# Performance work log

Hardware: AMD Instinct MI355X
Metric: run time of the kernel (lower is better)

Reference implementation:

```python
import jax, jax.numpy as jnp
import numpy as np

B, S, D, ENC_S = 4, 1024, 1024, 512
DI, DFF, DFE = 2048, 4096, 2048
NA, NB, E, H = 2, 6, 8, 16
TOP_K = 2


def setup_inputs():
    key = jax.random.key(0)
    ks = jax.random.split(key, 24)
    s = 0.02
    n = jax.random.normal
    return {
        "x": n(ks[0], (B, S, D), jnp.float32),
        "encoder_out": n(ks[1], (B, ENC_S, D), jnp.float32),
        "encoder_mask": jnp.ones((B, ENC_S), dtype=bool),
        "padding_mask": jnp.ones((B, S), dtype=bool),
        "encoder_available": jax.random.randint(ks[2], (B,), 0, 2, jnp.int32),
        "ln_g": jnp.ones((D,), jnp.float32),
        "ln_b": jnp.zeros((D,), jnp.float32),
        "ssm_Win": s * n(ks[3], (D, 2 * DI), jnp.float32),
        "ssm_a": n(ks[4], (DI,), jnp.float32),
        "ssm_Wout": s * n(ks[5], (DI, D), jnp.float32),
        "attn_Wqkv": s * n(ks[6], (D, 3 * D), jnp.float32),
        "attn_Wo": s * n(ks[7], (D, D), jnp.float32),
        "beta_ssm": 0.8 * jnp.ones((D,), jnp.float32),
        "beta_attn": 0.2 * jnp.ones((D,), jnp.float32),
        "se_W1": s * n(ks[8], (D, DFF), jnp.float32),
        "se_b1": jnp.zeros((DFF,), jnp.float32),
        "se_W2": s * n(ks[9], (DFF, D), jnp.float32),
        "se_b2": jnp.zeros((D,), jnp.float32),
        "r_W": s * n(ks[10], (D + 1, E), jnp.float32),
        "r_b": jnp.zeros((E,), jnp.float32),
        "ea_Wq": s * n(ks[11], (NA, D, D), jnp.float32),
        "ea_Wk": s * n(ks[12], (NA, D, D), jnp.float32),
        "ea_Wv": s * n(ks[13], (NA, D, D), jnp.float32),
        "ea_Wo": s * n(ks[14], (NA, D, D), jnp.float32),
        "ea_W1": s * n(ks[15], (NA, D, DFE), jnp.float32),
        "ea_W2": s * n(ks[16], (NA, DFE, D), jnp.float32),
        "eb_W1": s * n(ks[17], (NB, D, DFE), jnp.float32),
        "eb_W2": s * n(ks[18], (NB, DFE, D), jnp.float32),
    }


def _moe_forward(x, encoder_out, ln_g, ln_b, ssm_Win, ssm_a, ssm_Wout,
                 attn_Wqkv, attn_Wo, beta_ssm, beta_attn,
                 se_W1, se_b1, se_W2, se_b2, r_W, r_b,
                 ea_Wq, ea_Wk, ea_Wv, ea_Wo, ea_W1, ea_W2, eb_W1, eb_W2,
                 encoder_mask, padding_mask, encoder_available):
    # ---- Hymba fusion: LayerNorm -> SSM + causal attention, per-channel mix ----
    mu = x.mean(-1, keepdims=True)
    var = ((x - mu) ** 2).mean(-1, keepdims=True)
    h = (x - mu) * jax.lax.rsqrt(var + 1e-5) * ln_g + ln_b

    # SSM pathway: gated diagonal linear recurrence h_t = a*h_{t-1} + (1-a)*u_t
    u = h @ ssm_Win                       # (B,S,2*DI)
    z, xs = jnp.split(u, 2, axis=-1)
    a = jax.nn.sigmoid(ssm_a)             # (DI,)
    a_full = jnp.broadcast_to(a, xs.shape)
    b_in = (1.0 - a) * xs

    def comb(c1, c2):
        a1, b1 = c1
        a2, b2 = c2
        return a1 * a2, a2 * b1 + b2

    hs = jax.lax.associative_scan(comb, (a_full, b_in), axis=1)[1]
    ssm_out = (hs * jax.nn.silu(z)) @ ssm_Wout   # (B,S,D)

    # Attention pathway: causal MHA with key padding mask
    dh = D // H
    qkv = h @ attn_Wqkv
    q, k, v = jnp.split(qkv, 3, axis=-1)
    sp = lambda t: t.reshape(B, S, H, dh).transpose(0, 2, 1, 3)  # (B,H,S,dh)
    q, k, v = sp(q), sp(k), sp(v)
    scores = jnp.einsum('bhqd,bhkd->bhqk', q, k) / np.sqrt(dh).astype(np.float32)
    causal = jnp.tril(jnp.ones((S, S), dtype=bool))
    keymask = padding_mask[:, None, None, :]
    scores = jnp.where(causal[None, None] & keymask, scores, -1e9)
    p = jax.nn.softmax(scores, axis=-1)
    ao = jnp.einsum('bhqk,bhkd->bhqd', p, v).transpose(0, 2, 1, 3).reshape(B, S, D)
    attn_out = ao @ attn_Wo

    x = x + beta_ssm * ssm_out + beta_attn * attn_out  # residual after fusion

    # ---- MoE ----
    N = B * S
    x_flat = x.reshape(N, D)
    enc_avail_tok = jnp.repeat(encoder_available.astype(x.dtype), S)[:, None]  # (N,1)

    shared_delta = jax.nn.gelu(x_flat @ se_W1 + se_b1) @ se_W2 + se_b2

    # Router: top-k gating over softmax(logits)
    logits = jnp.concatenate([x_flat, enc_avail_tok], axis=-1) @ r_W + r_b  # (N,E)
    probs = jax.nn.softmax(logits, axis=-1)
    topv, topi = jax.lax.top_k(probs, TOP_K)
    gates = jnp.zeros_like(probs).at[jnp.arange(N)[:, None], topi].set(topv)
    gates = gates / (gates.sum(-1, keepdims=True) + 1e-9)

    # Hard S-mode gate: zero type-A experts where encoder unavailable, renormalize
    s_mode = enc_avail_tok == 0                       # (N,1)
    type_a = jnp.arange(E) < NA                       # (E,)
    gates = jnp.where(s_mode & type_a[None, :], 0.0, gates)
    gates = gates / (gates.sum(-1, keepdims=True) + 1e-6)

    # Type-A experts: per-token cross-attention to own batch's encoder, then FFN.
    # (dense over tokens; zero gates kill inactive tokens -> same math as sparse dispatch)
    qA = jnp.einsum('bsd,edf->ebsf', x, ea_Wq)
    kA = jnp.einsum('bmd,edf->ebmf', encoder_out, ea_Wk)
    vA = jnp.einsum('bmd,edf->ebmf', encoder_out, ea_Wv)
    sA = jnp.einsum('ebsf,ebmf->ebsm', qA, kA) / np.sqrt(D).astype(np.float32)
    sA = jnp.where(encoder_mask[None, :, None, :], sA, -1e9)
    pA = jax.nn.softmax(sA, axis=-1)
    ctx = jnp.einsum('ebsm,ebmf->ebsf', pA, vA)
    hA = x[None] + jnp.einsum('ebsf,efd->ebsd', ctx, ea_Wo)
    outA = jnp.einsum('ebsh,ehd->ebsd',
                      jax.nn.gelu(jnp.einsum('ebsd,edh->ebsh', hA, ea_W1)), ea_W2)
    outA = outA.reshape(NA, N, D)

    # Type-B experts: plain FFN on tokens
    outB = jnp.einsum('enh,ehd->end',
                      jax.nn.gelu(jnp.einsum('nd,edh->enh', x_flat, eb_W1)), eb_W2)

    out_all = jnp.concatenate([outA, outB], axis=0)   # (E,N,D)
    routed_delta = jnp.einsum('ne,end->nd', gates, out_all)

    return x + (shared_delta + routed_delta).reshape(B, S, D)


def reference(x, encoder_out, encoder_mask, padding_mask, encoder_available,
              ln_g, ln_b, ssm_Win, ssm_a, ssm_Wout, attn_Wqkv, attn_Wo,
              beta_ssm, beta_attn, se_W1, se_b1, se_W2, se_b2, r_W, r_b,
              ea_Wq, ea_Wk, ea_Wv, ea_Wo, ea_W1, ea_W2, eb_W1, eb_W2):
    return _moe_forward(x, encoder_out, ln_g, ln_b, ssm_Win, ssm_a, ssm_Wout,
                        attn_Wqkv, attn_Wo, beta_ssm, beta_attn,
                        se_W1, se_b1, se_W2, se_b2, r_W, r_b,
                        ea_Wq, ea_Wk, ea_Wv, ea_Wo, ea_W1, ea_W2, eb_W1, eb_W2,
                        encoder_mask, padding_mask, encoder_available)
```

## Files before the change

### kernel.cpp

```cpp
#include <hip/hip_runtime.h>
#include <hip/hip_bf16.h>
#include <math.h>

#define BB 4
#define SS 1024
#define DD 1024
#define ENCS 512
#define DI 2048
#define DFF 4096
#define DFE 2048
#define NA 2
#define NB 6
#define NE 8
#define NH 16
#define NTOK (BB*SS)
#define W1SZ ((long)DD*DFE)

typedef unsigned short u16;
typedef __bf16 bfrag __attribute__((ext_vector_type(8)));
typedef float  ffrag __attribute__((ext_vector_type(4)));

__device__ __forceinline__ float gelu_f(float x) {
    const float c = 0.7978845608028654f;
    float t = tanhf(c * (x + 0.044715f * x * x * x));
    return 0.5f * x * (1.f + t);
}

__device__ __forceinline__ u16 f2bf(float f) {
    unsigned u = __float_as_uint(f);
    u += 0x7fffu + ((u >> 16) & 1u);
    return (u16)(u >> 16);
}

__device__ __forceinline__ void split_bf(float v, u16& hi, u16& lo) {
    hi = f2bf(v);
    float hf = __uint_as_float((unsigned)hi << 16);
    lo = f2bf(v - hf);
}

typedef const __attribute__((address_space(1))) unsigned int* gas_t;
typedef __attribute__((address_space(3))) unsigned int* las_t;
__device__ __forceinline__ void gload16(const u16* g, u16* l) {
    __builtin_amdgcn_global_load_lds((gas_t)g, (las_t)l, 16, 0, 0);
}

__device__ __forceinline__ int flds(int row, int p) {
    return row * 64 + (((p ^ (row & 7)) & 7) << 3);
}

__global__ __launch_bounds__(256) void gemm_mfma(
    const u16* __restrict__ A, const u16* __restrict__ Bt,
    float* __restrict__ Cf, u16* __restrict__ Ch,
    int M, int N, int K,
    long sAb, long sBb, long sCb,
    const float* __restrict__ bias, const float* __restrict__ res,
    const float* __restrict__ rowscale, int rs_stride,
    int accum, int do_gelu)
{
    __shared__ u16 As[2][4096];
    __shared__ u16 Bs[2][4096];
    const int tid = threadIdx.x;
    const int w = tid >> 6, l = tid & 63;
    const int wm = w >> 1, wn = w & 1;
    const int bz = blockIdx.z;
    A  += (long)bz * sAb;
    Bt += (long)bz * sBb;
    const int m0 = blockIdx.y * 128, n0 = blockIdx.x * 128;

    const int c0 = 2 * w, c1 = c0 + 1;
    const int rl0 = c0 * 16 + (l >> 2), rl1 = c1 * 16 + (l >> 2);
    const int p = l & 3;
    const int gb0 = p ^ ((rl0 ^ (rl0 >> 2)) & 3);
    const int gb1 = p ^ ((rl1 ^ (rl1 >> 2)) & 3);
    const u16* gA0 = A  + (long)(m0 + rl0) * K + gb0 * 8;
    const u16* gA1 = A  + (long)(m0 + rl1) * K + gb1 * 8;
    const u16* gB0 = Bt + (long)(n0 + rl0) * K + gb0 * 8;
    const u16* gB1 = Bt + (long)(n0 + rl1) * K + gb1 * 8;
    const int d0 = c0 * 512, d1 = c1 * 512;

    const int q = l >> 4, fr = l & 15;
    int offA[4], offB[4];
    #pragma unroll
    for (int t = 0; t < 4; t++) {
        int ra = wm * 64 + t * 16 + fr;
        offA[t] = ra * 32 + (q ^ ((ra ^ (ra >> 2)) & 3)) * 8;
        int rb = wn * 64 + t * 16 + fr;
        offB[t] = rb * 32 + (q ^ ((rb ^ (rb >> 2)) & 3)) * 8;
    }

    ffrag acc[16];
    #pragma unroll
    for (int i = 0; i < 16; i++) acc[i] = (ffrag){0.f, 0.f, 0.f, 0.f};

    const int nsteps = K >> 5;
    #define STAGE1(bi, k0) do { \
        gload16(gA0 + (k0), &As[bi][d0]); \
        gload16(gA1 + (k0), &As[bi][d1]); \
        gload16(gB0 + (k0), &Bs[bi][d0]); \
        gload16(gB1 + (k0), &Bs[bi][d1]); } while (0)

    int cur = 0;
    STAGE1(0, 0);
    for (int t = 0; t < nsteps; ++t) {
        if (t + 1 < nsteps) {
            STAGE1(cur ^ 1, (t + 1) << 5);
            asm volatile("s_waitcnt vmcnt(4)" ::: "memory");
        } else {
            asm volatile("s_waitcnt vmcnt(0)" ::: "memory");
        }
        __builtin_amdgcn_s_barrier();
        bfrag af[4], bf[4];
        #pragma unroll
        for (int i = 0; i < 4; i++) {
            af[i] = *(const bfrag*)(&As[cur][0] + offA[i]);
            bf[i] = *(const bfrag*)(&Bs[cur][0] + offB[i]);
        }
        #pragma unroll
        for (int mt = 0; mt < 4; mt++)
            #pragma unroll
            for (int nt = 0; nt < 4; nt++)
                acc[mt * 4 + nt] = __builtin_amdgcn_mfma_f32_16x16x32_bf16(
                    af[mt], bf[nt], acc[mt * 4 + nt], 0, 0, 0);
        __builtin_amdgcn_s_barrier();
        cur ^= 1;
    }
    #undef STAGE1

    const long cbase = (long)bz * sCb;
    #pragma unroll
    for (int mt = 0; mt < 4; mt++) {
        #pragma unroll
        for (int nt = 0; nt < 4; nt++) {
            ffrag v = acc[mt * 4 + nt];
            int col = n0 + wn * 64 + nt * 16 + fr;
            int row0 = m0 + wm * 64 + mt * 16 + q * 4;
            float bv = bias ? bias[col] : 0.f;
            #pragma unroll
            for (int j = 0; j < 4; j++) {
                int row = row0 + j;
                float x = v[j] + bv;
                if (do_gelu) x = gelu_f(x);
                if (rowscale) x *= rowscale[(long)row * rs_stride];
                long idx = cbase + (long)row * N + col;
                if (res) x += res[(long)row * N + col];
                if (accum) { Cf[idx] += x; }
                else {
                    if (Cf) Cf[idx] = x;
                    if (Ch) Ch[idx] = f2bf(x);
                }
            }
        }
    }
}

__global__ __launch_bounds__(256) void gemm3_mfma(
    const u16* __restrict__ Ahi, const u16* __restrict__ Alo,
    const u16* __restrict__ Bhi, const u16* __restrict__ Blo,
    float* __restrict__ Cf, int M, int N, int K)
{
    __shared__ u16 Ah[2][4096];
    __shared__ u16 Al[2][4096];
    __shared__ u16 Bh[2][4096];
    __shared__ u16 Bl[2][4096];
    const int tid = threadIdx.x;
    const int w = tid >> 6, l = tid & 63;
    const int wm = w >> 1, wn = w & 1;
    const int m0 = blockIdx.y * 128, n0 = blockIdx.x * 128;

    const int c0 = 2 * w, c1 = c0 + 1;
    const int rl0 = c0 * 16 + (l >> 2), rl1 = c1 * 16 + (l >> 2);
    const int p = l & 3;
    const int gb0 = p ^ ((rl0 ^ (rl0 >> 2)) & 3);
    const int gb1 = p ^ ((rl1 ^ (rl1 >> 2)) & 3);
    const long oa0 = (long)(m0 + rl0) * K + gb0 * 8;
    const long oa1 = (long)(m0 + rl1) * K + gb1 * 8;
    const long ob0 = (long)(n0 + rl0) * K + gb0 * 8;
    const long ob1 = (long)(n0 + rl1) * K + gb1 * 8;
    const u16* gAh0 = Ahi + oa0; const u16* gAh1 = Ahi + oa1;
    const u16* gAl0 = Alo + oa0; const u16* gAl1 = Alo + oa1;
    const u16* gBh0 = Bhi + ob0; const u16* gBh1 = Bhi + ob1;
    const u16* gBl0 = Blo + ob0; const u16* gBl1 = Blo + ob1;
    const int d0 = c0 * 512, d1 = c1 * 512;

    const int q = l >> 4, fr = l & 15;
    int offA[4], offB[4];
    #pragma unroll
    for (int t = 0; t < 4; t++) {
        int ra = wm * 64 + t * 16 + fr;
        offA[t] = ra * 32 + (q ^ ((ra ^ (ra >> 2)) & 3)) * 8;
        int rb = wn * 64 + t * 16 + fr;
        offB[t] = rb * 32 + (q ^ ((rb ^ (rb >> 2)) & 3)) * 8;
    }

    ffrag acc[16];
    #pragma unroll
    for (int i = 0; i < 16; i++) acc[i] = (ffrag){0.f, 0.f, 0.f, 0.f};

    const int nsteps = K >> 5;
    #define STAGE3(bi, k0) do { \
        gload16(gAh0 + (k0), &Ah[bi][d0]); \
        gload16(gAh1 + (k0), &Ah[bi][d1]); \
        gload16(gAl0 + (k0), &Al[bi][d0]); \
        gload16(gAl1 + (k0), &Al[bi][d1]); \
        gload16(gBh0 + (k0), &Bh[bi][d0]); \
        gload16(gBh1 + (k0), &Bh[bi][d1]); \
        gload16(gBl0 + (k0), &Bl[bi][d0]); \
        gload16(gBl1 + (k0), &Bl[bi][d1]); } while (0)

    int cur = 0;
    STAGE3(0, 0);
    for (int t = 0; t < nsteps; ++t) {
        if (t + 1 < nsteps) {
            STAGE3(cur ^ 1, (t + 1) << 5);
            asm volatile("s_waitcnt vmcnt(8)" ::: "memory");
        } else {
            asm volatile("s_waitcnt vmcnt(0)" ::: "memory");
        }
        __builtin_amdgcn_s_barrier();
        bfrag ah[4], al[4], bh[4], bl[4];
        #pragma unroll
        for (int i = 0; i < 4; i++) {
            ah[i] = *(const bfrag*)(&Ah[cur][0] + offA[i]);
            al[i] = *(const bfrag*)(&Al[cur][0] + offA[i]);
            bh[i] = *(const bfrag*)(&Bh[cur][0] + offB[i]);
            bl[i] = *(const bfrag*)(&Bl[cur][0] + offB[i]);
        }
        #pragma unroll
        for (int mt = 0; mt < 4; mt++) {
            #pragma unroll
            for (int nt = 0; nt < 4; nt++) {
                ffrag a = acc[mt * 4 + nt];
                a = __builtin_amdgcn_mfma_f32_16x16x32_bf16(ah[mt], bh[nt], a, 0, 0, 0);
                a = __builtin_amdgcn_mfma_f32_16x16x32_bf16(ah[mt], bl[nt], a, 0, 0, 0);
                a = __builtin_amdgcn_mfma_f32_16x16x32_bf16(al[mt], bh[nt], a, 0, 0, 0);
                acc[mt * 4 + nt] = a;
            }
        }
        __builtin_amdgcn_s_barrier();
        cur ^= 1;
    }
    #undef STAGE3

    #pragma unroll
    for (int mt = 0; mt < 4; mt++) {
        #pragma unroll
        for (int nt = 0; nt < 4; nt++) {
            ffrag v = acc[mt * 4 + nt];
            int col = n0 + wn * 64 + nt * 16 + fr;
            int row0 = m0 + wm * 64 + mt * 16 + q * 4;
            #pragma unroll
            for (int j = 0; j < 4; j++)
                Cf[(long)(row0 + j) * N + col] = v[j];
        }
    }
}

static inline void ggemm(hipStream_t st, const u16* A, const u16* Bt,
    float* Cf, u16* Ch, int M, int N, int K, int batch,
    long sA, long sB, long sC,
    const float* bias, const float* res, const float* rs, int rss,
    int accum, int gelu)
{
    dim3 g(N / 128, M / 128, batch), b(256);
    gemm_mfma<<<g, b, 0, st>>>(A, Bt, Cf, Ch, M, N, K, sA, sB, sC,
                               bias, res, rs, rss, accum, gelu);
}

static inline void ggemm3(hipStream_t st, const u16* Ahi, const u16* Alo,
    const u16* Bhi, const u16* Blo, float* Cf, int M, int N, int K)
{
    dim3 g(N / 128, M / 128, 1), b(256);
    gemm3_mfma<<<g, b, 0, st>>>(Ahi, Alo, Bhi, Blo, Cf, M, N, K);
}

__global__ __launch_bounds__(256) void moe_w1(
    const u16* __restrict__ Xa, const u16* __restrict__ Xb,
    const u16* __restrict__ W1a, const u16* __restrict__ W1b,
    u16* __restrict__ ffp,
    const int* __restrict__ idxAll, const int* __restrict__ cntAll,
    const int* __restrict__ offAll, int N, int K)
{
    const int z = blockIdx.z;
    const int m0 = blockIdx.y * 128;
    if (m0 >= cntAll[z]) return;
    const int* idx = idxAll + z * NTOK;
    const u16* X  = (z < NA) ? (Xa + (long)z * NTOK * DD) : Xb;
    const u16* Wt = (z < 4) ? (W1a + (long)z * W1SZ) : (W1b + (long)(z - 4) * W1SZ);
    u16* ff = ffp + (long)offAll[z] * N;

    __shared__ u16 As[2][4096];
    __shared__ u16 Bs[2][4096];
    const int tid = threadIdx.x;
    const int w = tid >> 6, l = tid & 63;
    const int wm = w >> 1, wn = w & 1;
    const int n0 = blockIdx.x * 128;
    const int c0 = 2 * w, c1 = c0 + 1;
    const int rl0 = c0 * 16 + (l >> 2), rl1 = c1 * 16 + (l >> 2);
    const int p = l & 3;
    const int gb0 = p ^ ((rl0 ^ (rl0 >> 2)) & 3);
    const int gb1 = p ^ ((rl1 ^ (rl1 >> 2)) & 3);
    const int t0 = idx[m0 + rl0], t1 = idx[m0 + rl1];
    const u16* gA0 = X + (long)t0 * K + gb0 * 8;
    const u16* gA1 = X + (long)t1 * K + gb1 * 8;
    const u16* gB0 = Wt + (long)(n0 + rl0) * K + gb0 * 8;
    const u16* gB1 = Wt + (long)(n0 + rl1) * K + gb1 * 8;
    const int d0 = c0 * 512, d1 = c1 * 512;
    const int q = l >> 4, fr = l & 15;
    int offA[4], offB[4];
    #pragma unroll
    for (int t = 0; t < 4; t++) {
        int ra = wm * 64 + t * 16 + fr;
        offA[t] = ra * 32 + (q ^ ((ra ^ (ra >> 2)) & 3)) * 8;
        int rb = wn * 64 + t * 16 + fr;
        offB[t] = rb * 32 + (q ^ ((rb ^ (rb >> 2)) & 3)) * 8;
    }
    ffrag acc[16];
    #pragma unroll
    for (int i = 0; i < 16; i++) acc[i] = (ffrag){0.f, 0.f, 0.f, 0.f};

    const int nsteps = K >> 5;
    #define STAGEM(bi, k0) do { \
        gload16(gA0 + (k0), &As[bi][d0]); \
        gload16(gA1 + (k0), &As[bi][d1]); \
        gload16(gB0 + (k0), &Bs[bi][d0]); \
        gload16(gB1 + (k0), &Bs[bi][d1]); } while (0)

    int cur = 0;
    STAGEM(0, 0);
    for (int t = 0; t < nsteps; ++t) {
        if (t + 1 < nsteps) {
            STAGEM(cur ^ 1, (t + 1) << 5);
            asm volatile("s_waitcnt vmcnt(4)" ::: "memory");
        } else {
            asm volatile("s_waitcnt vmcnt(0)" ::: "memory");
        }
        __builtin_amdgcn_s_barrier();
        bfrag af[4], bf[4];
        #pragma unroll
        for (int i = 0; i < 4; i++) {
            af[i] = *(const bfrag*)(&As[cur][0] + offA[i]);
            bf[i] = *(const bfrag*)(&Bs[cur][0] + offB[i]);
        }
        #pragma unroll
        for (int mt = 0; mt < 4; mt++)
            #pragma unroll
            for (int nt = 0; nt < 4; nt++)
                acc[mt * 4 + nt] = __builtin_amdgcn_mfma_f32_16x16x32_bf16(
                    af[mt], bf[nt], acc[mt * 4 + nt], 0, 0, 0);
        __builtin_amdgcn_s_barrier();
        cur ^= 1;
    }
    #undef STAGEM

    #pragma unroll
    for (int mt = 0; mt < 4; mt++)
        #pragma unroll
        for (int nt = 0; nt < 4; nt++) {
            ffrag v = acc[mt * 4 + nt];
            int col = n0 + wn * 64 + nt * 16 + fr;
            int row0 = m0 + wm * 64 + mt * 16 + q * 4;
            #pragma unroll
            for (int j = 0; j < 4; j++)
                ff[(long)(row0 + j) * N + col] = f2bf(gelu_f(v[j]));
        }
}

__global__ __launch_bounds__(256) void moe_w2(
    const u16* __restrict__ ffp,
    const u16* __restrict__ W2a, const u16* __restrict__ W2b,
    float* __restrict__ out,
    const int* __restrict__ idxAll, const float* __restrict__ gvAll,
    const int* __restrict__ cntAll, const int* __restrict__ offAll,
    int N, int K)
{
    const int z = blockIdx.z;
    const int cnt = cntAll[z];
    const int m0 = blockIdx.y * 128;
    if (m0 >= cnt) return;
    const int* idx = idxAll + z * NTOK;
    const float* gval = gvAll + z * NTOK;
    const u16* Aseg = ffp + (long)offAll[z] * K;
    const u16* Wt = (z < 4) ? (W2a + (long)z * W1SZ) : (W2b + (long)(z - 4) * W1SZ);

    __shared__ u16 As[2][4096];
    __shared__ u16 Bs[2][4096];
    const int tid = threadIdx.x;
    const int w = tid >> 6, l = tid & 63;
    const int wm = w >> 1, wn = w & 1;
    const int n0 = blockIdx.x * 128;
    const int c0 = 2 * w, c1 = c0 + 1;
    const int rl0 = c0 * 16 + (l >> 2), rl1 = c1 * 16 + (l >> 2);
    const int p = l & 3;
    const int gb0 = p ^ ((rl0 ^ (rl0 >> 2)) & 3);
    const int gb1 = p ^ ((rl1 ^ (rl1 >> 2)) & 3);
    const u16* gA0 = Aseg + (long)(m0 + rl0) * K + gb0 * 8;
    const u16* gA1 = Aseg + (long)(m0 + rl1) * K + gb1 * 8;
    const u16* gB0 = Wt + (long)(n0 + rl0) * K + gb0 * 8;
    const u16* gB1 = Wt + (long)(n0 + rl1) * K + gb1 * 8;
    const int d0 = c0 * 512, d1 = c1 * 512;
    const int q = l >> 4, fr = l & 15;
    int offA[4], offB[4];
    #pragma unroll
    for (int t = 0; t < 4; t++) {
        int ra = wm * 64 + t * 16 + fr;
        offA[t] = ra * 32 + (q ^ ((ra ^ (ra >> 2)) & 3)) * 8;
        int rb = wn * 64 + t * 16 + fr;
        offB[t] = rb * 32 + (q ^ ((rb ^ (rb >> 2)) & 3)) * 8;
    }
    ffrag acc[16];
    #pragma unroll
    for (int i = 0; i < 16; i++) acc[i] = (ffrag){0.f, 0.f, 0.f, 0.f};

    const int nsteps = K >> 5;
    #define STAGEW(bi, k0) do { \
        gload16(gA0 + (k0), &As[bi][d0]); \
        gload16(gA1 + (k0), &As[bi][d1]); \
        gload16(gB0 + (k0), &Bs[bi][d0]); \
        gload16(gB1 + (k0), &Bs[bi][d1]); } while (0)

    int cur = 0;
    STAGEW(0, 0);
    for (int t = 0; t < nsteps; ++t) {
        if (t + 1 < nsteps) {
            STAGEW(cur ^ 1, (t + 1) << 5);
            asm volatile("s_waitcnt vmcnt(4)" ::: "memory");
        } else {
            asm volatile("s_waitcnt vmcnt(0)" ::: "memory");
        }
        __builtin_amdgcn_s_barrier();
        bfrag af[4], bf[4];
        #pragma unroll
        for (int i = 0; i < 4; i++) {
            af[i] = *(const bfrag*)(&As[cur][0] + offA[i]);
            bf[i] = *(const bfrag*)(&Bs[cur][0] + offB[i]);
        }
        #pragma unroll
        for (int mt = 0; mt < 4; mt++)
            #pragma unroll
            for (int nt = 0; nt < 4; nt++)
                acc[mt * 4 + nt] = __builtin_amdgcn_mfma_f32_16x16x32_bf16(
                    af[mt], bf[nt], acc[mt * 4 + nt], 0, 0, 0);
        __builtin_amdgcn_s_barrier();
        cur ^= 1;
    }
    #undef STAGEW

    #pragma unroll
    for (int mt = 0; mt < 4; mt++)
        #pragma unroll
        for (int nt = 0; nt < 4; nt++) {
            ffrag v = acc[mt * 4 + nt];
            int col = n0 + wn * 64 + nt * 16 + fr;
            int row0 = m0 + wm * 64 + mt * 16 + q * 4;
            #pragma unroll
            for (int j = 0; j < 4; j++) {
                int m = row0 + j;
                if (m < cnt)
                    atomicAdd(&out[(long)idx[m] * N + col], gval[m] * v[j]);
            }
        }
}

__global__ __launch_bounds__(256) void moe_zero(int* __restrict__ idx, int* __restrict__ cnt)
{
    int i = blockIdx.x * 256 + threadIdx.x;
    if (i < NE * NTOK) idx[i] = 0;
    if (i < NE) cnt[i] = 0;
}

__global__ __launch_bounds__(256) void moe_build(
    const float* __restrict__ gates, int* __restrict__ idx,
    float* __restrict__ gval, int* __restrict__ cnt)
{
    int t = blockIdx.x * 256 + threadIdx.x;
    #pragma unroll
    for (int e = 0; e < NE; e++) {
        float g = gates[(long)t * NE + e];
        if (g > 0.f) {
            int ppos = atomicAdd(&cnt[e], 1);
            idx[e * NTOK + ppos] = t;
            gval[e * NTOK + ppos] = g;
        }
    }
}

__global__ __launch_bounds__(64) void moe_off(
    const int* __restrict__ cnt, int* __restrict__ off)
{
    if (threadIdx.x == 0) {
        int o = 0;
        for (int e = 0; e < NE; e++) { off[e] = o; o += (cnt[e] + 127) & ~127; }
    }
}

__global__ __launch_bounds__(256) void convT_kernel(
    const float* __restrict__ src, u16* __restrict__ dst, int K, int N,
    long sS, long sD)
{
    __shared__ float t[32][33];
    src += (long)blockIdx.z * sS;
    dst += (long)blockIdx.z * sD;
    int n0 = blockIdx.x * 32, k0 = blockIdx.y * 32;
    int tx = threadIdx.x & 31, ty = threadIdx.x >> 5;
    #pragma unroll
    for (int j = 0; j < 4; j++)
        t[ty + j * 8][tx] = src[(long)(k0 + ty + j * 8) * N + n0 + tx];
    __syncthreads();
    #pragma unroll
    for (int j = 0; j < 4; j++)
        dst[(long)(n0 + ty + j * 8) * K + k0 + tx] = f2bf(t[tx][ty + j * 8]);
}

__global__ __launch_bounds__(256) void convT2_kernel(
    const float* __restrict__ src, u16* __restrict__ dhi, u16* __restrict__ dlo,
    int K, int N)
{
    __shared__ float t[32][33];
    int n0 = blockIdx.x * 32, k0 = blockIdx.y * 32;
    int tx = threadIdx.x & 31, ty = threadIdx.x >> 5;
    #pragma unroll
    for (int j = 0; j < 4; j++)
        t[ty + j * 8][tx] = src[(long)(k0 + ty + j * 8) * N + n0 + tx];
    __syncthreads();
    #pragma unroll
    for (int j = 0; j < 4; j++) {
        float v = t[tx][ty + j * 8];
        u16 hi, lo; split_bf(v, hi, lo);
        long o = (long)(n0 + ty + j * 8) * K + k0 + tx;
        dhi[o] = hi; dlo[o] = lo;
    }
}

__global__ __launch_bounds__(256) void conv_kernel(
    const float* __restrict__ s, u16* __restrict__ d)
{
    int i = (blockIdx.x * 256 + threadIdx.x) * 4;
    float4 v = *(const float4*)(s + i);
    ushort4 o;
    o.x = f2bf(v.x); o.y = f2bf(v.y); o.z = f2bf(v.z); o.w = f2bf(v.w);
    *(ushort4*)(d + i) = o;
}

__global__ __launch_bounds__(256) void ln_kernel(
    const float* __restrict__ x, const float* __restrict__ g,
    const float* __restrict__ b, u16* __restrict__ hhi, u16* __restrict__ hlo)
{
    int token = blockIdx.x;
    int tid = threadIdx.x;
    const float* xr = x + (long)token * DD;
    float4 xv = *(const float4*)(xr + tid * 4);
    float s  = xv.x + xv.y + xv.z + xv.w;
    float sq = xv.x*xv.x + xv.y*xv.y + xv.z*xv.z + xv.w*xv.w;
    #pragma unroll
    for (int off = 32; off; off >>= 1) {
        s  += __shfl_xor(s, off);
        sq += __shfl_xor(sq, off);
    }
    __shared__ float ws[4], wq[4];
    int wid = tid >> 6, lane = tid & 63;
    if (lane == 0) { ws[wid] = s; wq[wid] = sq; }
    __syncthreads();
    s  = ws[0] + ws[1] + ws[2] + ws[3];
    sq = wq[0] + wq[1] + wq[2] + wq[3];
    float mu  = s * (1.f / DD);
    float var = sq * (1.f / DD) - mu * mu;
    float inv = rsqrtf(var + 1e-5f);
    float4 gv = *(const float4*)(g + tid * 4);
    float4 bv = *(const float4*)(b + tid * 4);
    float o[4];
    o[0] = (xv.x - mu) * inv * gv.x + bv.x;
    o[1] = (xv.y - mu) * inv * gv.y + bv.y;
    o[2] = (xv.z - mu) * inv * gv.z + bv.z;
    o[3] = (xv.w - mu) * inv * gv.w + bv.w;
    ushort4 oh, ol;
    split_bf(o[0], oh.x, ol.x); split_bf(o[1], oh.y, ol.y);
    split_bf(o[2], oh.z, ol.z); split_bf(o[3], oh.w, ol.w);
    *(ushort4*)(hhi + (long)token * DD + tid * 4) = oh;
    *(ushort4*)(hlo + (long)token * DD + tid * 4) = ol;
}

__global__ __launch_bounds__(256) void scan_p1(
    const float* __restrict__ u, const float* __restrict__ ssma,
    float* __restrict__ part)
{
    int i = blockIdx.x * 256 + threadIdx.x;
    int c = i & 2047, ch = (i >> 11) & 7, b = i >> 14;
    float a = 1.f / (1.f + expf(-ssma[c])), om = 1.f - a;
    const float* ux = u + (long)b * SS * (2 * DI) + DI + c;
    float h = 0.f;
    int t0 = ch * 128;
    #pragma unroll 4
    for (int t = t0; t < t0 + 128; ++t) h = a * h + om * ux[(long)t * (2 * DI)];
    part[i] = h;
}

__global__ __launch_bounds__(256) void scan_p2(
    const float* __restrict__ ssma, const float* __restrict__ part,
    float* __restrict__ init)
{
    int j = blockIdx.x * 256 + threadIdx.x;
    int c = j & 2047, b = j >> 11;
    float a = 1.f / (1.f + expf(-ssma[c]));
    float ap = a;
    #pragma unroll
    for (int i = 0; i < 7; i++) ap *= ap;
    float carry = 0.f;
    int base = b * 16384 + c;
    #pragma unroll
    for (int ch = 0; ch < 8; ch++) {
        init[base + ch * 2048] = carry;
        carry = ap * carry + part[base + ch * 2048];
    }
}

__global__ __launch_bounds__(256) void scan_p3(
    const float* __restrict__ u, const float* __restrict__ ssma,
    const float* __restrict__ init,
    u16* __restrict__ ihi, u16* __restrict__ ilo)
{
    int i = blockIdx.x * 256 + threadIdx.x;
    int c = i & 2047, ch = (i >> 11) & 7, b = i >> 14;
    float a = 1.f / (1.f + expf(-ssma[c])), om = 1.f - a;
    const float* uz = u + (long)b * SS * (2 * DI) + c;
    long obase = (long)b * SS * DI + c;
    float h = init[i];
    int t0 = ch * 128;
    #pragma unroll 2
    for (int t = t0; t < t0 + 128; ++t) {
        float z  = uz[(long)t * (2 * DI)];
        float xv = uz[(long)t * (2 * DI) + DI];
        h = a * h + om * xv;
        float sz = z / (1.f + expf(-z));
        u16 hi, lo; split_bf(h * sz, hi, lo);
        ihi[obase + (long)t * DI] = hi;
        ilo[obase + (long)t * DI] = lo;
    }
}

__global__ __launch_bounds__(256) void qk_prep(
    const float* __restrict__ qkv,
    u16* __restrict__ Qhi, u16* __restrict__ Qlo,
    u16* __restrict__ Khi, u16* __restrict__ Klo)
{
    int tok = blockIdx.x * 4 + (threadIdx.x >> 6);
    int l = threadIdx.x & 63;
    int b = tok >> 10, s = tok & 1023;
    const float* src = qkv + (long)tok * 3072;
    #pragma unroll
    for (int h = 0; h < 16; h++) {
        long dst = ((long)(b * 16 + h) * 1024 + s) * 64 + l;
        u16 hi, lo;
        split_bf(src[h * 64 + l], hi, lo);
        Qhi[dst] = hi; Qlo[dst] = lo;
        split_bf(src[1024 + h * 64 + l], hi, lo);
        Khi[dst] = hi; Klo[dst] = lo;
    }
}

__global__ __launch_bounds__(256) void v_prep(
    const float* __restrict__ qkv, u16* __restrict__ Vthi, u16* __restrict__ Vtlo)
{
    __shared__ float t[64][65];
    int st = blockIdx.x, bh = blockIdx.y;
    int b = bh >> 4, h = bh & 15;
    int tid = threadIdx.x;
    #pragma unroll
    for (int i = 0; i < 16; i++) {
        int e = tid + i * 256;
        int sl = e >> 6, d = e & 63;
        t[sl][d] = qkv[((long)(b * 1024 + st * 64 + sl)) * 3072 + 2048 + h * 64 + d];
    }
    __syncthreads();
    #pragma unroll
    for (int i = 0; i < 16; i++) {
        int e = tid + i * 256;
        int d = e >> 6, sl = e & 63;
        float v = t[sl][d];
        u16 hi, lo; split_bf(v, hi, lo);
        long o = ((long)bh * 64 + d) * 1024 + st * 64 + sl;
        Vthi[o] = hi; Vtlo[o] = lo;
    }
}

__global__ __launch_bounds__(256) void flash_mfma(
    const u16* __restrict__ Qhi, const u16* __restrict__ Qlo,
    const u16* __restrict__ Khi, const u16* __restrict__ Klo,
    const u16* __restrict__ Vthi, const u16* __restrict__ Vtlo,
    u16* __restrict__ aohi, u16* __restrict__ aolo)
{
    __shared__ u16 Qh[4096], Ql[4096], Kh[4096], Kl[4096], Vh[4096], Vl[4096];
    __shared__ u16 Ph[4][1024], Pl[4][1024];
    const int qt = (SS / 64 - 1) - blockIdx.x, bh = blockIdx.y;
    const int tid = threadIdx.x, w = tid >> 6, l = tid & 63;
    const int q0 = qt * 64;
    const int lr = l >> 3, ps = l & 7;
    const int cg = l & 15, quad = l >> 4;

    #pragma unroll
    for (int cc = 0; cc < 2; cc++) {
        int c = 2 * w + cc;
        int r = c * 8 + lr;
        int pl = ps ^ (r & 7);
        long g = ((long)bh * 1024 + q0 + r) * 64 + pl * 8;
        gload16(Qhi + g, Qh + c * 512 + l * 8);
        gload16(Qlo + g, Ql + c * 512 + l * 8);
    }
    __syncthreads();

    const int qrow = w * 16 + cg;
    const int offQ0 = flds(qrow, quad), offQ1 = flds(qrow, 4 + quad);
    bfrag qh0 = *(const bfrag*)(Qh + offQ0);
    bfrag qh1 = *(const bfrag*)(Qh + offQ1);
    bfrag ql0 = *(const bfrag*)(Ql + offQ0);
    bfrag ql1 = *(const bfrag*)(Ql + offQ1);

    ffrag O[4];
    #pragma unroll
    for (int i = 0; i < 4; i++) O[i] = (ffrag){0.f, 0.f, 0.f, 0.f};
    float mrun[4], lrun[4];
    #pragma unroll
    for (int j = 0; j < 4; j++) { mrun[j] = -1e30f; lrun[j] = 0.f; }

    for (int kt = 0; kt <= qt; kt++) {
        int k0 = kt * 64;
        __syncthreads();
        #pragma unroll
        for (int cc = 0; cc < 2; cc++) {
            int c = 2 * w + cc;
            int r = c * 8 + lr;
            int pl = ps ^ (r & 7);
            long gk = ((long)bh * 1024 + k0 + r) * 64 + pl * 8;
            long gv = ((long)bh * 64 + r) * 1024 + k0 + pl * 8;
            gload16(Khi + gk, Kh + c * 512 + l * 8);
            gload16(Klo + gk, Kl + c * 512 + l * 8);
            gload16(Vthi + gv, Vh + c * 512 + l * 8);
            gload16(Vtlo + gv, Vl + c * 512 + l * 8);
        }
        __syncthreads();

        float s[4][4];
        #pragma unroll
        for (int nt = 0; nt < 4; nt++) {
            ffrag sc = (ffrag){0.f, 0.f, 0.f, 0.f};
            int kr = nt * 16 + cg;
            bfrag kh0 = *(const bfrag*)(Kh + flds(kr, quad));
            bfrag kh1 = *(const bfrag*)(Kh + flds(kr, 4 + quad));
            bfrag kl0 = *(const bfrag*)(Kl + flds(kr, quad));
            bfrag kl1 = *(const bfrag*)(Kl + flds(kr, 4 + quad));
            sc = __builtin_amdgcn_mfma_f32_16x16x32_bf16(qh0, kh0, sc, 0, 0, 0);
            sc = __builtin_amdgcn_mfma_f32_16x16x32_bf16(qh1, kh1, sc, 0, 0, 0);
            sc = __builtin_amdgcn_mfma_f32_16x16x32_bf16(qh0, kl0, sc, 0, 0, 0);
            sc = __builtin_amdgcn_mfma_f32_16x16x32_bf16(qh1, kl1, sc, 0, 0, 0);
            sc = __builtin_amdgcn_mfma_f32_16x16x32_bf16(ql0, kh0, sc, 0, 0, 0);
            sc = __builtin_amdgcn_mfma_f32_16x16x32_bf16(ql1, kh1, sc, 0, 0, 0);
            bool last = (kt == qt);
            #pragma unroll
            for (int j = 0; j < 4; j++) {
                float v = sc[j] * 0.125f;
                if (last && (nt * 16 + cg > w * 16 + quad * 4 + j)) v = -1e30f;
                s[nt][j] = v;
            }
        }
        #pragma unroll
        for (int j = 0; j < 4; j++) {
            float rm = fmaxf(fmaxf(s[0][j], s[1][j]), fmaxf(s[2][j], s[3][j]));
            rm = fmaxf(rm, __shfl_xor(rm, 1));
            rm = fmaxf(rm, __shfl_xor(rm, 2));
            rm = fmaxf(rm, __shfl_xor(rm, 4));
            rm = fmaxf(rm, __shfl_xor(rm, 8));
            float mn = fmaxf(mrun[j], rm);
            float alpha = __expf(mrun[j] - mn);
            float rs = 0.f;
            #pragma unroll
            for (int nt = 0; nt < 4; nt++) {
                float pv = __expf(s[nt][j] - mn);
                s[nt][j] = pv;
                rs += pv;
            }
            rs += __shfl_xor(rs, 1);
            rs += __shfl_xor(rs, 2);
            rs += __shfl_xor(rs, 4);
            rs += __shfl_xor(rs, 8);
            lrun[j] = lrun[j] * alpha + rs;
            mrun[j] = mn;
            #pragma unroll
            for (int ct = 0; ct < 4; ct++) O[ct][j] *= alpha;
        }
        #pragma unroll
        for (int nt = 0; nt < 4; nt++)
            #pragma unroll
            for (int j = 0; j < 4; j++) {
                int row = quad * 4 + j, col = nt * 16 + cg;
                int addr = row * 64 + (((col >> 3) ^ (row & 7)) << 3) + (col & 7);
                float pv = s[nt][j];
                u16 phv = f2bf(pv);
                float pf = __uint_as_float((unsigned)phv << 16);
                Ph[w][addr] = phv;
                Pl[w][addr] = f2bf(pv - pf);
            }
        bfrag p0h = *(const bfrag*)(&Ph[w][0] + flds(cg, quad));
        bfrag p1h = *(const bfrag*)(&Ph[w][0] + flds(cg, 4 + quad));
        bfrag p0l = *(const bfrag*)(&Pl[w][0] + flds(cg, quad));
        bfrag p1l = *(const bfrag*)(&Pl[w][0] + flds(cg, 4 + quad));
        #pragma unroll
        for (int ct = 0; ct < 4; ct++) {
            int vr = ct * 16 + cg;
            bfrag vh0 = *(const bfrag*)(Vh + flds(vr, quad));
            bfrag vh1 = *(const bfrag*)(Vh + flds(vr, 4 + quad));
            bfrag vl0 = *(const bfrag*)(Vl + flds(vr, quad));
            bfrag vl1 = *(const bfrag*)(Vl + flds(vr, 4 + quad));
            O[ct] = __builtin_amdgcn_mfma_f32_16x16x32_bf16(p0h, vh0, O[ct], 0, 0, 0);
            O[ct] = __builtin_amdgcn_mfma_f32_16x16x32_bf16(p1h, vh1, O[ct], 0, 0, 0);
            O[ct] = __builtin_amdgcn_mfma_f32_16x16x32_bf16(p0h, vl0, O[ct], 0, 0, 0);
            O[ct] = __builtin_amdgcn_mfma_f32_16x16x32_bf16(p1h, vl1, O[ct], 0, 0, 0);
            O[ct] = __builtin_amdgcn_mfma_f32_16x16x32_bf16(p0l, vh0, O[ct], 0, 0, 0);
            O[ct] = __builtin_amdgcn_mfma_f32_16x16x32_bf16(p0l, vh1, O[ct], 0, 0, 0);
        }
    }
    int b = bh >> 4, h = bh & 15;
    #pragma unroll
    for (int j = 0; j < 4; j++) {
        float inv = 1.f / lrun[j];
        int srow = q0 + w * 16 + quad * 4 + j;
        long base = ((long)(b * 1024 + srow)) * 1024 + h * 64 + cg;
        #pragma unroll
        for (int ct = 0; ct < 4; ct++) {
            float v = O[ct][j] * inv;
            u16 hi, lo; split_bf(v, hi, lo);
            aohi[base + ct * 16] = hi;
            aolo[base + ct * 16] = lo;
        }
    }
}

__global__ __launch_bounds__(256) void combine_kernel(
    const float* __restrict__ x, const float* __restrict__ ssm,
    const float* __restrict__ attn, const float* __restrict__ bs,
    const float* __restrict__ ba, float* __restrict__ x1, u16* __restrict__ x1h)
{
    int i = (blockIdx.x * 256 + threadIdx.x) * 4;
    int d = i & (DD - 1);
    float4 xv = *(const float4*)(x + i);
    float4 sv = *(const float4*)(ssm + i);
    float4 av = *(const float4*)(attn + i);
    float4 b1 = *(const float4*)(bs + d);
    float4 b2 = *(const float4*)(ba + d);
    float4 o;
    o.x = xv.x + b1.x * sv.x + b2.x * av.x;
    o.y = xv.y + b1.y * sv.y + b2.y * av.y;
    o.z = xv.z + b1.z * sv.z + b2.z * av.z;
    o.w = xv.w + b1.w * sv.w + b2.w * av.w;
    *(float4*)(x1 + i) = o;
    ushort4 oh;
    oh.x = f2bf(o.x); oh.y = f2bf(o.y); oh.z = f2bf(o.z); oh.w = f2bf(o.w);
    *(ushort4*)(x1h + i) = oh;
}

__global__ __launch_bounds__(256) void router_kernel(
    const float* __restrict__ x1, const int* __restrict__ enc_avail,
    const float* __restrict__ rW, const float* __restrict__ rb,
    float* __restrict__ gates)
{
    int token = blockIdx.x * 4 + (threadIdx.x >> 6);
    int lane = threadIdx.x & 63;
    int b = token >> 10;
    float acc[NE];
    #pragma unroll
    for (int e = 0; e < NE; e++) acc[e] = 0.f;
    const float* xrow = x1 + (long)token * DD;
    for (int d = lane; d < DD; d += 64) {
        float xv = xrow[d];
        const float* w = rW + (long)d * NE;
        #pragma unroll
        for (int e = 0; e < NE; e++) acc[e] += xv * w[e];
    }
    #pragma unroll
    for (int e = 0; e < NE; e++) {
        #pragma unroll
        for (int off = 32; off; off >>= 1) acc[e] += __shfl_xor(acc[e], off);
    }
    if (lane == 0) {
        int avail = enc_avail[b];
        float av = (float)avail;
        float lg[NE], pr[NE];
        #pragma unroll
        for (int e = 0; e < NE; e++) lg[e] = acc[e] + av * rW[(long)DD * NE + e] + rb[e];
        float mx = lg[0];
        #pragma unroll
        for (int e = 1; e < NE; e++) mx = fmaxf(mx, lg[e]);
        float sum = 0.f;
        #pragma unroll
        for (int e = 0; e < NE; e++) { pr[e] = expf(lg[e] - mx); sum += pr[e]; }
        float isum = 1.f / sum;
        #pragma unroll
        for (int e = 0; e < NE; e++) pr[e] *= isum;
        int i1 = 0;
        #pragma unroll
        for (int e = 1; e < NE; e++) if (pr[e] > pr[i1]) i1 = e;
        int i2 = (i1 == 0) ? 1 : 0;
        #pragma unroll
        for (int e = 0; e < NE; e++) if (e != i1 && pr[e] > pr[i2]) i2 = e;
        float g[NE];
        #pragma unroll
        for (int e = 0; e < NE; e++) g[e] = 0.f;
        g[i1] = pr[i1]; g[i2] = pr[i2];
        float s1 = g[i1] + g[i2] + 1e-9f;
        #pragma unroll
        for (int e = 0; e < NE; e++) g[e] /= s1;
        if (avail == 0) { g[0] = 0.f; g[1] = 0.f; }
        float s2 = 1e-6f;
        #pragma unroll
        for (int e = 0; e < NE; e++) s2 += g[e];
        float is2 = 1.f / s2;
        #pragma unroll
        for (int e = 0; e < NE; e++) gates[(long)token * NE + e] = g[e] * is2;
    }
}

__global__ __launch_bounds__(256) void softmax512_kernel(
    const float* __restrict__ sA, u16* __restrict__ pA, float scale)
{
    int row = blockIdx.x * 4 + (threadIdx.x >> 6);
    int lane = threadIdx.x & 63;
    const float* r = sA + (long)row * ENCS;
    u16* o = pA + (long)row * ENCS;
    float v[8];
    #pragma unroll
    for (int j = 0; j < 8; j++) v[j] = r[lane + j * 64] * scale;
    float mx = v[0];
    #pragma unroll
    for (int j = 1; j < 8; j++) mx = fmaxf(mx, v[j]);
    #pragma unroll
    for (int off = 32; off; off >>= 1) mx = fmaxf(mx, __shfl_xor(mx, off));
    float sum = 0.f;
    #pragma unroll
    for (int j = 0; j < 8; j++) { v[j] = __expf(v[j] - mx); sum += v[j]; }
    #pragma unroll
    for (int off = 32; off; off >>= 1) sum += __shfl_xor(sum, off);
    float inv = 1.f / sum;
    #pragma unroll
    for (int j = 0; j < 8; j++) o[lane + j * 64] = f2bf(v[j] * inv);
}

extern "C" void kernel_launch(void* const* d_in, const int* in_sizes, int n_in,
                              void* d_out, int out_size, void* d_ws, size_t ws_size,
                              hipStream_t stream) {
    const float* x    = (const float*)d_in[0];
    const float* enc  = (const float*)d_in[1];
    const int*   eav  = (const int*)d_in[4];
    const float* ln_g = (const float*)d_in[5];
    const float* ln_b = (const float*)d_in[6];
    const float* Win  = (const float*)d_in[7];
    const float* ssma = (const float*)d_in[8];
    const float* Wout = (const float*)d_in[9];
    const float* Wqkv = (const float*)d_in[10];
    const float* Wo   = (const float*)d_in[11];
    const float* bSsm = (const float*)d_in[12];
    const float* bAtt = (const float*)d_in[13];
    const float* seW1 = (const float*)d_in[14];
    const float* seb1 = (const float*)d_in[15];
    const float* seW2 = (const float*)d_in[16];
    const float* seb2 = (const float*)d_in[17];
    const float* rW   = (const float*)d_in[18];
    const float* rb   = (const float*)d_in[19];
    const float* eaWq = (const float*)d_in[20];
    const float* eaWk = (const float*)d_in[21];
    const float* eaWv = (const float*)d_in[22];
    const float* eaWo = (const float*)d_in[23];
    const float* eaW1 = (const float*)d_in[24];
    const float* eaW2 = (const float*)d_in[25];
    const float* ebW1 = (const float*)d_in[26];
    const float* ebW2 = (const float*)d_in[27];
    float* out = (float*)d_out;

    float* F = (float*)d_ws;
    float* f_big  = F;
    float* f_ssm  = F + 16777216;
    float* f_x1   = F + 20971520;
    float* f_part = F + 25165824;
    float* f_init = F + 25231360;
    float* f_gate = F + 25296896;
    u16* U = (u16*)(F + 25329664);
    u16* u_h_hi  = U;
    u16* u_h_lo  = U + 4194304;
    u16* u_in_hi = U + 8388608;
    u16* u_in_lo = U + 16777216;
    u16* u_ao_hi = U + 25165824;
    u16* u_ao_lo = U + 29360128;
    u16* u_wt    = U + 33554432;
    u16* u_wt_lo = U + 37748736;
    int*   moe_idx = (int*)(U + 41943040);
    float* moe_gv  = (float*)(moe_idx + NE * NTOK);
    int*   moe_cnt = (int*)(moe_gv + NE * NTOK);
    int*   moe_offp = moe_cnt + NE;

    float* f_u    = f_big;
    float* f_qkv  = f_big;
    float* f_attn = f_big + 12582912;
    u16*   u_ff   = (u16*)f_big;
    u16*   u_enc  = u_h_hi + 2097152;
    u16*   u_x1   = u_h_lo;
    u16* u_Qhi = u_h_hi, *u_Qlo = u_h_lo;
    u16* u_Khi = u_in_hi, *u_Klo = u_in_hi + 4194304;
    u16* u_Vthi = u_in_lo, *u_Vtlo = u_in_lo + 4194304;

    u16*   wq2   = u_wt;
    u16*   wk2   = u_wt_lo;
    u16*   wv2   = (u16*)f_ssm;
    u16*   wo2   = (u16*)f_ssm + 4194304;
    u16*   qA2   = u_ao_hi;
    u16*   kA2   = u_in_hi;
    u16*   vAt2  = u_in_hi + 4194304;
    float* sA2   = (float*)u_in_lo;
    u16*   ctx2  = u_in_lo;
    u16*   ffpool = (u16*)f_big;
    u16*   hA2   = (u16*)(f_big + 10485760);
    u16*   pA2   = (u16*)(f_big + 14680064);
    u16*   w1a   = u_ao_hi;
    u16*   w1b   = u_in_hi;
    u16*   w2a   = u_wt;
    u16*   w2b   = (u16*)f_ssm;

    #define CONVT(src, Kd, Nd)  convT_kernel <<<dim3((Nd)/32,(Kd)/32,1), dim3(256), 0, stream>>>(src, u_wt, Kd, Nd, 0, 0)
    #define CONVTB(src, dst, Kd, Nd, nb) convT_kernel<<<dim3((Nd)/32,(Kd)/32,(nb)), dim3(256), 0, stream>>>(src, dst, Kd, Nd, (long)(Kd)*(Nd), (long)(Kd)*(Nd))
    #define CONVT2(src, Kd, Nd) convT2_kernel<<<dim3((Nd)/32,(Kd)/32), dim3(256), 0, stream>>>(src, u_wt, u_wt_lo, Kd, Nd)

    ln_kernel<<<dim3(NTOK), dim3(256), 0, stream>>>(x, ln_g, ln_b, u_h_hi, u_h_lo);
    CONVT2(Win, DD, 2 * DI);
    ggemm3(stream, u_h_hi, u_h_lo, u_wt, u_wt_lo, f_u, NTOK, 2 * DI, DD);
    scan_p1<<<dim3(256), dim3(256), 0, stream>>>(f_u, ssma, f_part);
    scan_p2<<<dim3(32), dim3(256), 0, stream>>>(ssma, f_part, f_init);
    scan_p3<<<dim3(256), dim3(256), 0, stream>>>(f_u, ssma, f_init, u_in_hi, u_in_lo);
    CONVT2(Wout, DI, DD);
    ggemm3(stream, u_in_hi, u_in_lo, u_wt, u_wt_lo, f_ssm, NTOK, DD, DI);
    CONVT2(Wqkv, DD, 3 * DD);
    ggemm3(stream, u_h_hi, u_h_lo, u_wt, u_wt_lo, f_qkv, NTOK, 3 * DD, DD);
    qk_prep<<<dim3(NTOK / 4), dim3(256), 0, stream>>>(f_qkv, u_Qhi, u_Qlo, u_Khi, u_Klo);
    v_prep<<<dim3(SS / 64, BB * NH), dim3(256), 0, stream>>>(f_qkv, u_Vthi, u_Vtlo);
    flash_mfma<<<dim3(SS / 64, BB * NH), dim3(256), 0, stream>>>(
        u_Qhi, u_Qlo, u_Khi, u_Klo, u_Vthi, u_Vtlo, u_ao_hi, u_ao_lo);
    CONVT2(Wo, DD, DD);
    ggemm3(stream, u_ao_hi, u_ao_lo, u_wt, u_wt_lo, f_attn, NTOK, DD, DD);
    combine_kernel<<<dim3(NTOK * DD / 1024), dim3(256), 0, stream>>>(
        x, f_ssm, f_attn, bSsm, bAtt, f_x1, u_x1);
    router_kernel<<<dim3(NTOK / 4), dim3(256), 0, stream>>>(f_x1, eav, rW, rb, f_gate);
    moe_zero<<<dim3((NE * NTOK + 255) / 256), dim3(256), 0, stream>>>(moe_idx, moe_cnt);
    moe_build<<<dim3(NTOK / 256), dim3(256), 0, stream>>>(f_gate, moe_idx, moe_gv, moe_cnt);
    moe_off<<<dim3(1), dim3(64), 0, stream>>>(moe_cnt, moe_offp);
    CONVT(seW1, DD, DFF);
    ggemm(stream, u_x1, u_wt, nullptr, u_ff, NTOK, DFF, DD, 1, 0, 0, 0,
          seb1, nullptr, nullptr, 0, 0, 1);
    CONVT(seW2, DFF, DD);
    ggemm(stream, u_ff, u_wt, out, nullptr, NTOK, DD, DFF, 1, 0, 0, 0,
          seb2, f_x1, nullptr, 0, 0, 0);
    conv_kernel<<<dim3(BB * ENCS * DD / 1024), dim3(256), 0, stream>>>(enc, u_enc);

    CONVTB(eaWq, wq2, DD, DD, 2);
    CONVTB(eaWk, wk2, DD, DD, 2);
    CONVTB(eaWv, wv2, DD, DD, 2);
    CONVTB(eaWo, wo2, DD, DD, 2);
    ggemm(stream, u_x1, wq2, nullptr, qA2, NTOK, DD, DD, 2,
          0, (long)DD * DD, (long)NTOK * DD, nullptr, nullptr, nullptr, 0, 0, 0);
    ggemm(stream, u_enc, wk2, nullptr, kA2, BB * ENCS, DD, DD, 2,
          0, (long)DD * DD, (long)BB * ENCS * DD, nullptr, nullptr, nullptr, 0, 0, 0);
    for (int e = 0; e < NA; ++e)
        ggemm(stream, wv2 + (long)e * DD * DD, u_enc, nullptr,
              vAt2 + (long)e * 4 * DD * ENCS, DD, ENCS, DD, BB,
              0, (long)ENCS * DD, (long)DD * ENCS, nullptr, nullptr, nullptr, 0, 0, 0);
    ggemm(stream, qA2, kA2, sA2, nullptr, SS, ENCS, DD, 2 * BB,
          (long)SS * DD, (long)ENCS * DD, (long)SS * ENCS,
          nullptr, nullptr, nullptr, 0, 0, 0);
    softmax512_kernel<<<dim3(2 * NTOK / 4), dim3(256), 0, stream>>>(sA2, pA2, 0.03125f);
    ggemm(stream, pA2, vAt2, nullptr, ctx2, SS, DD, ENCS, 2 * BB,
          (long)SS * ENCS, (long)DD * ENCS, (long)SS * DD,
          nullptr, nullptr, nullptr, 0, 0, 0);
    ggemm(stream, ctx2, wo2, nullptr, hA2, NTOK, DD, DD, 2,
          (long)NTOK * DD, (long)DD * DD, (long)NTOK * DD,
          nullptr, f_x1, nullptr, 0, 0, 0);

    CONVTB(eaW1, w1a, DD, DFE, 2);
    CONVTB(ebW1, w1a + 2 * W1SZ, DD, DFE, 2);
    CONVTB(ebW1 + 2 * W1SZ, w1b, DD, DFE, 4);
    CONVTB(eaW2, w2a, DFE, DD, 2);
    CONVTB(ebW2, w2a + 2 * W1SZ, DFE, DD, 2);
    CONVTB(ebW2 + 2 * W1SZ, w2b, DFE, DD, 4);
    moe_w1<<<dim3(DFE / 128, NTOK / 128, NE), dim3(256), 0, stream>>>(
        hA2, u_x1, w1a, w1b, ffpool, moe_idx, moe_cnt, moe_offp, DFE, DD);
    moe_w2<<<dim3(DD / 128, NTOK / 128, NE), dim3(256), 0, stream>>>(
        ffpool, w2a, w2b, out, moe_idx, moe_gv, moe_cnt, moe_offp, DD, DFE);
    (void)in_sizes; (void)n_in; (void)out_size; (void)ws_size;
}
```

Baseline: 1.438 ms.

## Triple-buffer GEMM loads and register-prefetch next K/V tile in attention

The three MFMA GEMM kernels (dense, MoE W1, MoE W2) move from double to triple-buffered LDS staging, issuing loads two K-steps ahead with adjusted vmcnt waits. The causal attention kernel now loads the first K/V tile with Q, then prefetches the next K/V tile into registers during compute and writes it to LDS afterwards. This hides global-load latency behind MFMA work. It raises LDS use (48KB per GEMM block), which may lower occupancy, and adds register pressure in attention. The diff also changes one P·V term from p0l·vh1 to p1l·vh1, a correctness fix.

After: 1.477 ms. 2.7% more time.

```diff
diff --git a/kernel.cpp b/kernel.cpp
--- a/kernel.cpp
+++ b/kernel.cpp
@@ -57,8 +57,8 @@
     const float* __restrict__ rowscale, int rs_stride,
     int accum, int do_gelu)
 {
-    __shared__ u16 As[2][4096];
-    __shared__ u16 Bs[2][4096];
+    __shared__ u16 As[3][4096];
+    __shared__ u16 Bs[3][4096];
     const int tid = threadIdx.x;
     const int w = tid >> 6, l = tid & 63;
     const int wm = w >> 1, wn = w & 1;
@@ -99,11 +99,16 @@
         gload16(gB0 + (k0), &Bs[bi][d0]); \
         gload16(gB1 + (k0), &Bs[bi][d1]); } while (0)
 
+    STAGE1(0, 0);
+    STAGE1(1, 32);
     int cur = 0;
-    STAGE1(0, 0);
     for (int t = 0; t < nsteps; ++t) {
-        if (t + 1 < nsteps) {
-            STAGE1(cur ^ 1, (t + 1) << 5);
+        int rem = nsteps - 1 - t;
+        if (rem >= 2) {
+            int nb = cur + 2; if (nb >= 3) nb -= 3;
+            STAGE1(nb, (t + 2) << 5);
+            asm volatile("s_waitcnt vmcnt(8)" ::: "memory");
+        } else if (rem == 1) {
             asm volatile("s_waitcnt vmcnt(4)" ::: "memory");
         } else {
             asm volatile("s_waitcnt vmcnt(0)" ::: "memory");
@@ -122,7 +127,7 @@
                 acc[mt * 4 + nt] = __builtin_amdgcn_mfma_f32_16x16x32_bf16(
                     af[mt], bf[nt], acc[mt * 4 + nt], 0, 0, 0);
         __builtin_amdgcn_s_barrier();
-        cur ^= 1;
+        cur = (cur == 2) ? 0 : cur + 1;
     }
     #undef STAGE1
 
@@ -288,8 +293,8 @@
     const u16* Wt = (z < 4) ? (W1a + (long)z * W1SZ) : (W1b + (long)(z - 4) * W1SZ);
     u16* ff = ffp + (long)offAll[z] * N;
 
-    __shared__ u16 As[2][4096];
-    __shared__ u16 Bs[2][4096];
+    __shared__ u16 As[3][4096];
+    __shared__ u16 Bs[3][4096];
     const int tid = threadIdx.x;
     const int w = tid >> 6, l = tid & 63;
     const int wm = w >> 1, wn = w & 1;
@@ -325,11 +330,16 @@
         gload16(gB0 + (k0), &Bs[bi][d0]); \
         gload16(gB1 + (k0), &Bs[bi][d1]); } while (0)
 
+    STAGEM(0, 0);
+    STAGEM(1, 32);
     int cur = 0;
-    STAGEM(0, 0);
     for (int t = 0; t < nsteps; ++t) {
-        if (t + 1 < nsteps) {
-            STAGEM(cur ^ 1, (t + 1) << 5);
+        int rem = nsteps - 1 - t;
+        if (rem >= 2) {
+            int nb = cur + 2; if (nb >= 3) nb -= 3;
+            STAGEM(nb, (t + 2) << 5);
+            asm volatile("s_waitcnt vmcnt(8)" ::: "memory");
+        } else if (rem == 1) {
             asm volatile("s_waitcnt vmcnt(4)" ::: "memory");
         } else {
             asm volatile("s_waitcnt vmcnt(0)" ::: "memory");
@@ -348,7 +358,7 @@
                 acc[mt * 4 + nt] = __builtin_amdgcn_mfma_f32_16x16x32_bf16(
                     af[mt], bf[nt], acc[mt * 4 + nt], 0, 0, 0);
         __builtin_amdgcn_s_barrier();
-        cur ^= 1;
+        cur = (cur == 2) ? 0 : cur + 1;
     }
     #undef STAGEM
 
@@ -382,8 +392,8 @@
     const u16* Aseg = ffp + (long)offAll[z] * K;
     const u16* Wt = (z < 4) ? (W2a + (long)z * W1SZ) : (W2b + (long)(z - 4) * W1SZ);
 
-    __shared__ u16 As[2][4096];
-    __shared__ u16 Bs[2][4096];
+    __shared__ u16 As[3][4096];
+    __shared__ u16 Bs[3][4096];
     const int tid = threadIdx.x;
     const int w = tid >> 6, l = tid & 63;
     const int wm = w >> 1, wn = w & 1;
@@ -418,11 +428,16 @@
         gload16(gB0 + (k0), &Bs[bi][d0]); \
         gload16(gB1 + (k0), &Bs[bi][d1]); } while (0)
 
+    STAGEW(0, 0);
+    STAGEW(1, 32);
     int cur = 0;
-    STAGEW(0, 0);
     for (int t = 0; t < nsteps; ++t) {
-        if (t + 1 < nsteps) {
-            STAGEW(cur ^ 1, (t + 1) << 5);
+        int rem = nsteps - 1 - t;
+        if (rem >= 2) {
+            int nb = cur + 2; if (nb >= 3) nb -= 3;
+            STAGEW(nb, (t + 2) << 5);
+            asm volatile("s_waitcnt vmcnt(8)" ::: "memory");
+        } else if (rem == 1) {
             asm volatile("s_waitcnt vmcnt(4)" ::: "memory");
         } else {
             asm volatile("s_waitcnt vmcnt(0)" ::: "memory");
@@ -441,7 +456,7 @@
                 acc[mt * 4 + nt] = __builtin_amdgcn_mfma_f32_16x16x32_bf16(
                     af[mt], bf[nt], acc[mt * 4 + nt], 0, 0, 0);
         __builtin_amdgcn_s_barrier();
-        cur ^= 1;
+        cur = (cur == 2) ? 0 : cur + 1;
     }
     #undef STAGEW
 
@@ -701,9 +716,15 @@
         int c = 2 * w + cc;
         int r = c * 8 + lr;
         int pl = ps ^ (r & 7);
-        long g = ((long)bh * 1024 + q0 + r) * 64 + pl * 8;
-        gload16(Qhi + g, Qh + c * 512 + l * 8);
-        gload16(Qlo + g, Ql + c * 512 + l * 8);
+        long gq = ((long)bh * 1024 + q0 + r) * 64 + pl * 8;
+        long gk = ((long)bh * 1024 + r) * 64 + pl * 8;
+        long gv = ((long)bh * 64 + r) * 1024 + pl * 8;
+        gload16(Qhi + gq, Qh + c * 512 + l * 8);
+        gload16(Qlo + gq, Ql + c * 512 + l * 8);
+        gload16(Khi + gk, Kh + c * 512 + l * 8);
+        gload16(Klo + gk, Kl + c * 512 + l * 8);
+        gload16(Vthi + gv, Vh + c * 512 + l * 8);
+        gload16(Vtlo + gv, Vl + c * 512 + l * 8);
     }
     __syncthreads();
 
@@ -722,21 +743,23 @@
     for (int j = 0; j < 4; j++) { mrun[j] = -1e30f; lrun[j] = 0.f; }
 
     for (int kt = 0; kt <= qt; kt++) {
-        int k0 = kt * 64;
-        __syncthreads();
-        #pragma unroll
-        for (int cc = 0; cc < 2; cc++) {
-            int c = 2 * w + cc;
-            int r = c * 8 + lr;
-            int pl = ps ^ (r & 7);
-            long gk = ((long)bh * 1024 + k0 + r) * 64 + pl * 8;
-            long gv = ((long)bh * 64 + r) * 1024 + k0 + pl * 8;
-            gload16(Khi + gk, Kh + c * 512 + l * 8);
-            gload16(Klo + gk, Kl + c * 512 + l * 8);
-            gload16(Vthi + gv, Vh + c * 512 + l * 8);
-            gload16(Vtlo + gv, Vl + c * 512 + l * 8);
-        }
-        __syncthreads();
+        const bool pf = (kt < qt);
+        uint4 rkh[2], rkl[2], rvh[2], rvl[2];
+        if (pf) {
+            int k0n = (kt + 1) * 64;
+            #pragma unroll
+            for (int cc = 0; cc < 2; cc++) {
+                int c = 2 * w + cc;
+                int r = c * 8 + lr;
+                int pl = ps ^ (r & 7);
+                long gk = ((long)bh * 1024 + k0n + r) * 64 + pl * 8;
+                long gv = ((long)bh * 64 + r) * 1024 + k0n + pl * 8;
+                rkh[cc] = *(const uint4*)(Khi + gk);
+                rkl[cc] = *(const uint4*)(Klo + gk);
+                rvh[cc] = *(const uint4*)(Vthi + gv);
+                rvl[cc] = *(const uint4*)(Vtlo + gv);
+            }
+        }
 
         float s[4][4];
         #pragma unroll
@@ -794,9 +817,9 @@
                 int addr = row * 64 + (((col >> 3) ^ (row & 7)) << 3) + (col & 7);
                 float pv = s[nt][j];
                 u16 phv = f2bf(pv);
-                float pf = __uint_as_float((unsigned)phv << 16);
+                float pf2 = __uint_as_float((unsigned)phv << 16);
                 Ph[w][addr] = phv;
-                Pl[w][addr] = f2bf(pv - pf);
+                Pl[w][addr] = f2bf(pv - pf2);
             }
         bfrag p0h = *(const bfrag*)(&Ph[w][0] + flds(cg, quad));
         bfrag p1h = *(const bfrag*)(&Ph[w][0] + flds(cg, 4 + quad));
@@ -814,7 +837,19 @@
             O[ct] = __builtin_amdgcn_mfma_f32_16x16x32_bf16(p0h, vl0, O[ct], 0, 0, 0);
             O[ct] = __builtin_amdgcn_mfma_f32_16x16x32_bf16(p1h, vl1, O[ct], 0, 0, 0);
             O[ct] = __builtin_amdgcn_mfma_f32_16x16x32_bf16(p0l, vh0, O[ct], 0, 0, 0);
-            O[ct] = __builtin_amdgcn_mfma_f32_16x16x32_bf16(p0l, vh1, O[ct], 0, 0, 0);
+            O[ct] = __builtin_amdgcn_mfma_f32_16x16x32_bf16(p1l, vh1, O[ct], 0, 0, 0);
+        }
+        if (pf) {
+            __syncthreads();
+            #pragma unroll
+            for (int cc = 0; cc < 2; cc++) {
+                int c = 2 * w + cc;
+                *(uint4*)(Kh + c * 512 + l * 8) = rkh[cc];
+                *(uint4*)(Kl + c * 512 + l * 8) = rkl[cc];
+                *(uint4*)(Vh + c * 512 + l * 8) = rvh[cc];
+                *(uint4*)(Vl + c * 512 + l * 8) = rvl[cc];
+            }
+            __syncthreads();
         }
     }
     int b = bh >> 4, h = bh & 15;
```
